# Kernel tuning notes

Measured on AMD Instinct MI355X. Metric: run time of the kernel, lower is better.

The kernel has to match this reference:

```python
import jax, jax.numpy as jnp
import numpy as np

N = 50000
E = 800000
IN_C = 128
HID = 64
HEADS = 4
OUT_C = 64


def setup_inputs() -> dict:
    key = jax.random.key(0)
    ks = jax.random.split(key, 20)
    s = 0.05
    inp = {
        "x": jax.random.normal(ks[0], (N, IN_C), dtype=jnp.float32),
        "edge_index": jax.random.randint(ks[1], (2, E), 0, N, dtype=jnp.int64),
        # layer 0: in=128 -> heads=4, C=64
        "W0": jax.random.normal(ks[2], (IN_C, HEADS * HID), jnp.float32) * s,
        "a0s": jax.random.normal(ks[3], (HEADS, HID), jnp.float32) * s,
        "a0d": jax.random.normal(ks[4], (HEADS, HID), jnp.float32) * s,
        "b0": jnp.zeros((HEADS * HID,), jnp.float32),
        # layer 1: 256 -> heads=4, C=64
        "W1": jax.random.normal(ks[5], (HEADS * HID, HEADS * HID), jnp.float32) * s,
        "a1s": jax.random.normal(ks[6], (HEADS, HID), jnp.float32) * s,
        "a1d": jax.random.normal(ks[7], (HEADS, HID), jnp.float32) * s,
        "b1": jnp.zeros((HEADS * HID,), jnp.float32),
        # layer 2: 256 -> heads=1, C=64
        "W2": jax.random.normal(ks[8], (HEADS * HID, HID), jnp.float32) * s,
        "a2s": jax.random.normal(ks[9], (1, HID), jnp.float32) * s,
        "a2d": jax.random.normal(ks[10], (1, HID), jnp.float32) * s,
        "b2": jnp.zeros((HID,), jnp.float32),
        # prediction head: Linear(64 -> 64)
        "hw": jax.random.normal(ks[11], (HID, OUT_C), jnp.float32) * s,
        "hb": jnp.zeros((OUT_C,), jnp.float32),
    }
    return inp


def gat_conv(x, src, dst, W, a_s, a_d, b, heads, n_nodes):
    # x: [N, F_in]; returns [N, heads*C]
    C = a_s.shape[1]
    h = (x @ W).reshape(n_nodes, heads, C)          # [N,H,C]
    alpha_s = jnp.sum(h * a_s, axis=-1)             # [N,H]
    alpha_d = jnp.sum(h * a_d, axis=-1)             # [N,H]
    e = jax.nn.leaky_relu(alpha_s[src] + alpha_d[dst], negative_slope=0.2)  # [E,H]
    m = jax.ops.segment_max(e, dst, num_segments=n_nodes)                  # per-dst max
    ex = jnp.exp(e - m[dst])
    denom = jax.ops.segment_sum(ex, dst, num_segments=n_nodes)
    alpha = ex / (denom[dst] + 1e-16)               # [E,H]
    out = jax.ops.segment_sum(alpha[:, :, None] * h[src], dst, num_segments=n_nodes)
    return out.reshape(n_nodes, heads * C) + b


def reference(x, edge_index, W0, a0s, a0d, b0, W1, a1s, a1d, b1, W2, a2s, a2d, b2, hw, hb):
    n = x.shape[0]
    # PyG GATConv default add_self_loops=True
    loop = jnp.arange(n, dtype=edge_index.dtype)
    src = jnp.concatenate([edge_index[0], loop])
    dst = jnp.concatenate([edge_index[1], loop])

    h = gat_conv(x, src, dst, W0, a0s, a0d, b0, HEADS, n)
    h = jax.nn.relu(h)
    h = gat_conv(h, src, dst, W1, a1s, a1d, b1, HEADS, n)
    h = jax.nn.relu(h)
    h = gat_conv(h, src, dst, W2, a2s, a2d, b2, 1, n)
    # batch is None -> mean over all nodes, keepdim
    g = jnp.mean(h, axis=0, keepdims=True)          # [1, HID]
    return g @ hw + hb                               # [1, OUT_C]
```

## Files before the change

### kernel.cpp

```cpp
#include <hip/hip_runtime.h>
#include <hip/hip_bf16.h>
#include <cstddef>

#define NN 50000
#define EE 800000
#define NB ((NN + 255) / 256)

typedef __attribute__((ext_vector_type(8))) short short8;
typedef __attribute__((ext_vector_type(4))) float f32x4;

__device__ __forceinline__ float leaky(float x) { return x >= 0.f ? x : 0.2f * x; }
__device__ __forceinline__ float bf2f(unsigned short u) {
  return __uint_as_float(((unsigned int)u) << 16);
}
__device__ __forceinline__ float bflo(unsigned int v) { return __uint_as_float(v << 16); }
__device__ __forceinline__ float bfhi(unsigned int v) { return __uint_as_float(v & 0xFFFF0000u); }
__device__ __forceinline__ unsigned short f2bf(float f) {
  __hip_bfloat16 b = __float2bfloat16(f);
  return __builtin_bit_cast(unsigned short, b);
}
__device__ __forceinline__ float selh(float4 v, int h) {
  float a = (h & 1) ? v.y : v.x;
  float b = (h & 1) ? v.w : v.z;
  return (h & 2) ? b : a;
}
__device__ __forceinline__ void accum8(float a, uint4 v, float* acc) {
  acc[0] += a * bflo(v.x); acc[1] += a * bfhi(v.x);
  acc[2] += a * bflo(v.y); acc[3] += a * bfhi(v.y);
  acc[4] += a * bflo(v.z); acc[5] += a * bfhi(v.z);
  acc[6] += a * bflo(v.w); acc[7] += a * bfhi(v.w);
}

__global__ __launch_bounds__(256) void gemm_bf16_k(const unsigned short* __restrict__ A,
                                                   const unsigned short* __restrict__ Bt,
                                                   unsigned short* __restrict__ Cb,
                                                   int K, int Nfull,
                                                   const float* __restrict__ a_s,
                                                   const float* __restrict__ a_d,
                                                   float* __restrict__ als,
                                                   float* __restrict__ ald,
                                                   float* __restrict__ selfex) {
  __shared__ __align__(16) unsigned short As[128 * 40];
  __shared__ __align__(16) unsigned short Bs[64 * 40];
  const int tid = threadIdx.x;
  const int lane = tid & 63;
  const int w = tid >> 6;
  const int bm = blockIdx.x * 128;
  const int bn = blockIdx.y * 64;
  const int quad = lane >> 4;
  const int l16 = lane & 15;
  f32x4 acc[2][4] = {};
  for (int kc = 0; kc < K; kc += 32) {
    {
      int row = tid >> 2, seg = tid & 3;
      int sr = bm + row; if (sr >= NN) sr = NN - 1;
      *(uint4*)&As[row * 40 + seg * 8] = *(const uint4*)(A + (size_t)sr * K + kc + seg * 8);
      row = (tid + 256) >> 2; seg = (tid + 256) & 3;
      sr = bm + row; if (sr >= NN) sr = NN - 1;
      *(uint4*)&As[row * 40 + seg * 8] = *(const uint4*)(A + (size_t)sr * K + kc + seg * 8);
      int n = tid >> 2; seg = tid & 3;
      *(uint4*)&Bs[n * 40 + seg * 8] = *(const uint4*)(Bt + (size_t)(bn + n) * K + kc + seg * 8);
    }
    __syncthreads();
    short8 afr0 = *(const short8*)&As[(w * 32 + l16) * 40 + quad * 8];
    short8 afr1 = *(const short8*)&As[(w * 32 + 16 + l16) * 40 + quad * 8];
#pragma unroll
    for (int nt = 0; nt < 4; ++nt) {
      short8 bfr = *(const short8*)&Bs[(nt * 16 + l16) * 40 + quad * 8];
      acc[0][nt] = __builtin_amdgcn_mfma_f32_16x16x32_bf16(afr0, bfr, acc[0][nt], 0, 0, 0);
      acc[1][nt] = __builtin_amdgcn_mfma_f32_16x16x32_bf16(afr1, bfr, acc[1][nt], 0, 0, 0);
    }
    __syncthreads();
  }
  const int head = bn >> 6;
  const int Hmul = Nfull >> 6;
  float vs[2][4] = {};
  float vd[2][4] = {};
#pragma unroll
  for (int nt = 0; nt < 4; ++nt) {
    const float asv = a_s[head * 64 + nt * 16 + l16];
    const float adv = a_d[head * 64 + nt * 16 + l16];
#pragma unroll
    for (int mt = 0; mt < 2; ++mt)
#pragma unroll
      for (int reg = 0; reg < 4; ++reg) {
        unsigned short c = f2bf(acc[mt][nt][reg]);
        int r = bm + w * 32 + mt * 16 + quad * 4 + reg;
        if (r < NN) Cb[(size_t)r * Nfull + bn + nt * 16 + l16] = c;
        float hv = bf2f(c);
        vs[mt][reg] += hv * asv;
        vd[mt][reg] += hv * adv;
      }
  }
#pragma unroll
  for (int off = 1; off < 16; off <<= 1) {
#pragma unroll
    for (int mt = 0; mt < 2; ++mt)
#pragma unroll
      for (int reg = 0; reg < 4; ++reg) {
        vs[mt][reg] += __shfl_xor(vs[mt][reg], off, 64);
        vd[mt][reg] += __shfl_xor(vd[mt][reg], off, 64);
      }
  }
  if (l16 == 0) {
#pragma unroll
    for (int mt = 0; mt < 2; ++mt)
#pragma unroll
      for (int reg = 0; reg < 4; ++reg) {
        int r = bm + w * 32 + mt * 16 + quad * 4 + reg;
        if (r < NN) {
          als[(size_t)r * Hmul + head] = vs[mt][reg];
          ald[(size_t)r * Hmul + head] = vd[mt][reg];
          selfex[(size_t)r * Hmul + head] = __expf(leaky(vs[mt][reg] + vd[mt][reg]));
        }
      }
  }
}

__global__ __launch_bounds__(256) void hist_k(const int* __restrict__ ei, int* deg) {
  int i = blockIdx.x * 256 + threadIdx.x;
  if (i < EE) atomicAdd(&deg[ei[EE + i]], 1);
}

__global__ __launch_bounds__(256) void scan1_k(const int* __restrict__ deg,
                                               int* __restrict__ incl,
                                               int* __restrict__ partial) {
  __shared__ int s[256];
  int t = threadIdx.x;
  int i = blockIdx.x * 256 + t;
  int v = (i < NN) ? deg[i] : 0;
  s[t] = v;
  __syncthreads();
  for (int off = 1; off < 256; off <<= 1) {
    int u = (t >= off) ? s[t - off] : 0;
    __syncthreads();
    s[t] += u;
    __syncthreads();
  }
  if (i < NN) incl[i] = s[t];
  if (t == 255) partial[blockIdx.x] = s[255];
}

__global__ void scan2_k(int* __restrict__ partial) {
  __shared__ int s[256];
  int t = threadIdx.x;
  int v = (t < NB) ? partial[t] : 0;
  s[t] = v;
  __syncthreads();
  for (int off = 1; off < 256; off <<= 1) {
    int u = (t >= off) ? s[t - off] : 0;
    __syncthreads();
    s[t] += u;
    __syncthreads();
  }
  if (t < NB) partial[t] = s[t] - v;
}

__global__ __launch_bounds__(256) void scan3_k(const int* __restrict__ deg,
                                               const int* __restrict__ incl,
                                               const int* __restrict__ partial,
                                               int* __restrict__ rowptr,
                                               int* __restrict__ cursor) {
  int i = blockIdx.x * 256 + threadIdx.x;
  if (i >= NN) return;
  int r = partial[blockIdx.x] + incl[i] - deg[i];
  rowptr[i] = r;
  cursor[i] = r;
}

__global__ __launch_bounds__(256) void scatter_k(const int* __restrict__ ei,
                                                 int* __restrict__ cursor,
                                                 int* __restrict__ csr_src,
                                                 int* __restrict__ csr_dst) {
  int i = blockIdx.x * 256 + threadIdx.x;
  if (i >= EE) return;
  int d = ei[EE + i];
  int p = atomicAdd(&cursor[d], 1);
  csr_src[p] = ei[i];
  csr_dst[p] = d;
}

__global__ __launch_bounds__(256) void edge_exp4_k(const int* __restrict__ csr_src,
                                                   const int* __restrict__ csr_dst,
                                                   const float* __restrict__ als,
                                                   const float* __restrict__ ald,
                                                   float4* __restrict__ ex4) {
  int i = blockIdx.x * 256 + threadIdx.x;
  if (i >= EE) return;
  int s = csr_src[i], d = csr_dst[i];
  const float4 as4 = *(const float4*)(als + (size_t)s * 4);
  const float4 ad4 = *(const float4*)(ald + (size_t)d * 4);
  float4 e;
  e.x = __expf(leaky(as4.x + ad4.x));
  e.y = __expf(leaky(as4.y + ad4.y));
  e.z = __expf(leaky(as4.z + ad4.z));
  e.w = __expf(leaky(as4.w + ad4.w));
  ex4[i] = e;
}

__global__ __launch_bounds__(256) void edge_exp1_k(const int* __restrict__ csr_src,
                                                   const int* __restrict__ csr_dst,
                                                   const float* __restrict__ als,
                                                   const float* __restrict__ ald,
                                                   float* __restrict__ ex1) {
  int i = blockIdx.x * 256 + threadIdx.x;
  if (i >= EE) return;
  ex1[i] = __expf(leaky(als[csr_src[i]] + ald[csr_dst[i]]));
}

__global__ __launch_bounds__(256) void aggr4c_k(const int* __restrict__ rowptr,
                                                const int* __restrict__ deg,
                                                const int* __restrict__ csr_src,
                                                const float4* __restrict__ ex4,
                                                const float* __restrict__ selfex,
                                                const uint4* __restrict__ hb4,
                                                const float* __restrict__ bias,
                                                uint4* __restrict__ out4) {
  const int dst = blockIdx.x * 4 + (threadIdx.x >> 6);
  const int lane = threadIdx.x & 63;
  const int slot = lane >> 4;
  const int l16 = lane & 15;
  const int head = l16 >> 2;
  const int rs = rowptr[dst];
  const int dg = deg[dst];

  float acc[16] = {};
  float dsum = 0.f;
  if (slot == 0) {
    float a = selfex[dst * 4 + head];
    dsum += a;
    uint4 v0 = hb4[(size_t)dst * 32 + l16 * 2];
    uint4 v1 = hb4[(size_t)dst * 32 + l16 * 2 + 1];
    accum8(a, v0, acc);
    accum8(a, v1, acc + 8);
  }
  int j = slot;
  for (; j + 4 < dg; j += 8) {
    int s0 = csr_src[rs + j];
    int s1 = csr_src[rs + j + 4];
    float4 av0 = ex4[rs + j];
    float4 av1 = ex4[rs + j + 4];
    uint4 va0 = hb4[(size_t)s0 * 32 + l16 * 2];
    uint4 vb0 = hb4[(size_t)s0 * 32 + l16 * 2 + 1];
    uint4 va1 = hb4[(size_t)s1 * 32 + l16 * 2];
    uint4 vb1 = hb4[(size_t)s1 * 32 + l16 * 2 + 1];
    float a0 = selh(av0, head);
    float a1 = selh(av1, head);
    dsum += a0 + a1;
    accum8(a0, va0, acc);
    accum8(a0, vb0, acc + 8);
    accum8(a1, va1, acc);
    accum8(a1, vb1, acc + 8);
  }
  for (; j < dg; j += 4) {
    int s0 = csr_src[rs + j];
    float4 av0 = ex4[rs + j];
    uint4 va0 = hb4[(size_t)s0 * 32 + l16 * 2];
    uint4 vb0 = hb4[(size_t)s0 * 32 + l16 * 2 + 1];
    float a0 = selh(av0, head);
    dsum += a0;
    accum8(a0, va0, acc);
    accum8(a0, vb0, acc + 8);
  }
#pragma unroll
  for (int k = 0; k < 16; ++k) {
    acc[k] += __shfl_xor(acc[k], 16, 64);
    acc[k] += __shfl_xor(acc[k], 32, 64);
  }
  dsum += __shfl_xor(dsum, 16, 64);
  dsum += __shfl_xor(dsum, 32, 64);
  if (slot == 0) {
    const float inv = 1.f / (dsum + 1e-16f);
    const float* bz = bias + l16 * 16;
    uint4 o0, o1;
    float c0, c1;
    c0 = fmaxf(acc[0] * inv + bz[0], 0.f);   c1 = fmaxf(acc[1] * inv + bz[1], 0.f);
    o0.x = ((unsigned int)f2bf(c1) << 16) | f2bf(c0);
    c0 = fmaxf(acc[2] * inv + bz[2], 0.f);   c1 = fmaxf(acc[3] * inv + bz[3], 0.f);
    o0.y = ((unsigned int)f2bf(c1) << 16) | f2bf(c0);
    c0 = fmaxf(acc[4] * inv + bz[4], 0.f);   c1 = fmaxf(acc[5] * inv + bz[5], 0.f);
    o0.z = ((unsigned int)f2bf(c1) << 16) | f2bf(c0);
    c0 = fmaxf(acc[6] * inv + bz[6], 0.f);   c1 = fmaxf(acc[7] * inv + bz[7], 0.f);
    o0.w = ((unsigned int)f2bf(c1) << 16) | f2bf(c0);
    c0 = fmaxf(acc[8] * inv + bz[8], 0.f);   c1 = fmaxf(acc[9] * inv + bz[9], 0.f);
    o1.x = ((unsigned int)f2bf(c1) << 16) | f2bf(c0);
    c0 = fmaxf(acc[10] * inv + bz[10], 0.f); c1 = fmaxf(acc[11] * inv + bz[11], 0.f);
    o1.y = ((unsigned int)f2bf(c1) << 16) | f2bf(c0);
    c0 = fmaxf(acc[12] * inv + bz[12], 0.f); c1 = fmaxf(acc[13] * inv + bz[13], 0.f);
    o1.z = ((unsigned int)f2bf(c1) << 16) | f2bf(c0);
    c0 = fmaxf(acc[14] * inv + bz[14], 0.f); c1 = fmaxf(acc[15] * inv + bz[15], 0.f);
    o1.w = ((unsigned int)f2bf(c1) << 16) | f2bf(c0);
    out4[(size_t)dst * 32 + l16 * 2] = o0;
    out4[(size_t)dst * 32 + l16 * 2 + 1] = o1;
  }
}

__global__ __launch_bounds__(256) void aggr1c_k(const int* __restrict__ rowptr,
                                                const int* __restrict__ deg,
                                                const int* __restrict__ csr_src,
                                                const float* __restrict__ ex1,
                                                const float* __restrict__ selfex,
                                                const uint4* __restrict__ hb4,
                                                const float* __restrict__ bias,
                                                float* __restrict__ out) {
  const int dst = blockIdx.x * 4 + (threadIdx.x >> 6);
  const int lane = threadIdx.x & 63;
  const int slot = lane >> 3;
  const int c8 = lane & 7;
  const int rs = rowptr[dst];
  const int dg = deg[dst];

  float acc[8] = {};
  float dsum = 0.f;
  if (slot == 0) {
    float a = selfex[dst];
    dsum += a;
    uint4 v = hb4[(size_t)dst * 8 + c8];
    accum8(a, v, acc);
  }
  for (int j = slot; j < dg; j += 8) {
    int s = csr_src[rs + j];
    float a = ex1[rs + j];
    dsum += a;
    uint4 v = hb4[(size_t)s * 8 + c8];
    accum8(a, v, acc);
  }
#pragma unroll
  for (int k = 0; k < 8; ++k) {
    acc[k] += __shfl_xor(acc[k], 8, 64);
    acc[k] += __shfl_xor(acc[k], 16, 64);
    acc[k] += __shfl_xor(acc[k], 32, 64);
  }
  dsum += __shfl_xor(dsum, 8, 64);
  dsum += __shfl_xor(dsum, 16, 64);
  dsum += __shfl_xor(dsum, 32, 64);
  if (slot == 0) {
    const float inv = 1.f / (dsum + 1e-16f);
    const float4 bz0 = *(const float4*)(bias + c8 * 8);
    const float4 bz1 = *(const float4*)(bias + c8 * 8 + 4);
    float4 o0 = make_float4(acc[0] * inv + bz0.x, acc[1] * inv + bz0.y,
                            acc[2] * inv + bz0.z, acc[3] * inv + bz0.w);
    float4 o1 = make_float4(acc[4] * inv + bz1.x, acc[5] * inv + bz1.y,
                            acc[6] * inv + bz1.z, acc[7] * inv + bz1.w);
    *(float4*)(out + (size_t)dst * 64 + c8 * 8) = o0;
    *(float4*)(out + (size_t)dst * 64 + c8 * 8 + 4) = o1;
  }
}

__global__ __launch_bounds__(256) void castx_k(const float2* __restrict__ x2,
                                               unsigned int* __restrict__ xb_u) {
  int i = blockIdx.x * 256 + threadIdx.x;
  if (i >= NN * 64) return;
  float2 v = x2[i];
  xb_u[i] = ((unsigned int)f2bf(v.y) << 16) | f2bf(v.x);
}

__global__ __launch_bounds__(64) void trw_k(const float* __restrict__ W,
                                            unsigned short* __restrict__ Wt, int K, int N) {
  int k = blockIdx.x;
  int n = blockIdx.y * 64 + threadIdx.x;
  Wt[(size_t)n * K + k] = f2bf(W[(size_t)k * N + n]);
}

__global__ __launch_bounds__(256) void colsum_k(const float* __restrict__ h2,
                                                float* __restrict__ g) {
  __shared__ float s[256];
  int tid = threadIdx.x;
  int c = tid & 63, rg = tid >> 6;
  float acc = 0.f;
  for (int n = blockIdx.x * 4 + rg; n < NN; n += gridDim.x * 4)
    acc += h2[n * 64 + c];
  s[tid] = acc;
  __syncthreads();
  if (tid < 64) atomicAdd(&g[c], s[c] + s[64 + c] + s[128 + c] + s[192 + c]);
}

__global__ void head_k(const float* __restrict__ g, const float* __restrict__ hw,
                       const float* __restrict__ hb, float* __restrict__ out) {
  int o = threadIdx.x;
  float acc = 0.f;
  const float invN = 1.0f / (float)NN;
#pragma unroll 8
  for (int c = 0; c < 64; ++c) acc += (g[c] * invN) * hw[c * 64 + o];
  out[o] = acc + hb[o];
}

extern "C" void kernel_launch(void* const* d_in, const int* in_sizes, int n_in,
                              void* d_out, int out_size, void* d_ws, size_t ws_size,
                              hipStream_t stream) {
  const float* x   = (const float*)d_in[0];
  const int*   ei  = (const int*)d_in[1];
  const float* W0  = (const float*)d_in[2];
  const float* a0s = (const float*)d_in[3];
  const float* a0d = (const float*)d_in[4];
  const float* b0  = (const float*)d_in[5];
  const float* W1  = (const float*)d_in[6];
  const float* a1s = (const float*)d_in[7];
  const float* a1d = (const float*)d_in[8];
  const float* b1  = (const float*)d_in[9];
  const float* W2  = (const float*)d_in[10];
  const float* a2s = (const float*)d_in[11];
  const float* a2d = (const float*)d_in[12];
  const float* b2  = (const float*)d_in[13];
  const float* hw  = (const float*)d_in[14];
  const float* hb  = (const float*)d_in[15];
  float* out = (float*)d_out;

  char* w = (char*)d_ws;
  unsigned short* xb   = (unsigned short*)w; w += (size_t)NN * 128 * 2;
  unsigned short* bufG = (unsigned short*)w; w += (size_t)NN * 256 * 2;
  unsigned short* bufA = (unsigned short*)w; w += (size_t)NN * 256 * 2;
  float* bufF = (float*)w;                   w += (size_t)NN * 64 * 4;
  unsigned short* W0t = (unsigned short*)w;  w += 256 * 128 * 2;
  unsigned short* W1t = (unsigned short*)w;  w += 256 * 256 * 2;
  unsigned short* W2t = (unsigned short*)w;  w += 64 * 256 * 2;
  float* als  = (float*)w;    w += (size_t)NN * 4 * 4;
  float* ald  = (float*)w;    w += (size_t)NN * 4 * 4;
  float* sfx  = (float*)w;    w += (size_t)NN * 4 * 4;
  float4* ex4 = (float4*)w;   w += (size_t)EE * 16;
  int* deg     = (int*)w;     w += (size_t)NN * 4;
  int* rowptr  = (int*)w;     w += (size_t)NN * 4;
  int* cursor  = (int*)w;     w += (size_t)NN * 4;
  int* incl    = (int*)w;     w += (size_t)NN * 4;
  int* partial = (int*)w;     w += 256 * 4;
  int* csr_src = (int*)w;     w += (size_t)EE * 4;
  int* csr_dst = (int*)w;     w += (size_t)EE * 4;
  float* g    = (float*)w;    w += 256;

  hipMemsetAsync(deg, 0, (size_t)NN * 4, stream);
  hist_k<<<(EE + 255) / 256, 256, 0, stream>>>(ei, deg);
  scan1_k<<<NB, 256, 0, stream>>>(deg, incl, partial);
  scan2_k<<<1, 256, 0, stream>>>(partial);
  scan3_k<<<NB, 256, 0, stream>>>(deg, incl, partial, rowptr, cursor);
  scatter_k<<<(EE + 255) / 256, 256, 0, stream>>>(ei, cursor, csr_src, csr_dst);

  castx_k<<<(NN * 64 + 255) / 256, 256, 0, stream>>>((const float2*)x, (unsigned int*)xb);
  trw_k<<<dim3(128, 4), 64, 0, stream>>>(W0, W0t, 128, 256);
  trw_k<<<dim3(256, 4), 64, 0, stream>>>(W1, W1t, 256, 256);
  trw_k<<<dim3(256, 1), 64, 0, stream>>>(W2, W2t, 256, 64);

  const int GX = (NN + 127) / 128;
  const int GA = NN / 4;
  const int GE = EE / 256;

  auto layer4 = [&](const unsigned short* in, int K, const unsigned short* Wt,
                    const float* a_s, const float* a_d, const float* bias,
                    unsigned short* hbuf, unsigned short* obuf) {
    gemm_bf16_k<<<dim3(GX, 4), 256, 0, stream>>>(in, Wt, hbuf, K, 256,
                                                 a_s, a_d, als, ald, sfx);
    edge_exp4_k<<<GE, 256, 0, stream>>>(csr_src, csr_dst, als, ald, ex4);
    aggr4c_k<<<GA, 256, 0, stream>>>(rowptr, deg, csr_src, ex4, sfx,
                                     (const uint4*)hbuf, bias, (uint4*)obuf);
  };

  layer4(xb, 128, W0t, a0s, a0d, b0, bufG, bufA);
  layer4(bufA, 256, W1t, a1s, a1d, b1, bufG, bufA);

  gemm_bf16_k<<<dim3(GX, 1), 256, 0, stream>>>(bufA, W2t, bufG, 256, 64,
                                               a2s, a2d, als, ald, sfx);
  edge_exp1_k<<<GE, 256, 0, stream>>>(csr_src, csr_dst, als, ald, (float*)ex4);
  aggr1c_k<<<GA, 256, 0, stream>>>(rowptr, deg, csr_src, (const float*)ex4, sfx,
                                   (const uint4*)bufG, b2, bufF);

  hipMemsetAsync(g, 0, 64 * 4, stream);
  colsum_k<<<256, 256, 0, stream>>>(bufF, g);
  head_k<<<1, 64, 0, stream>>>(g, hw, hb, out);
}
```

Measured before the change: 451.6 us.

## Deepen gather unrolling in aggregation kernels and fuse prep and head launches

Unrolls the 4-head aggregation loop from 2 to 4 edges per iteration and the 1-head loop from 1 to 2 edges, so more independent gathers are in flight per wave. Merges the x cast and three weight-transpose kernels into one prep kernel. Folds the final head matmul into the column-sum kernel using a last-block-done atomic counter, which removes launches at the cost of more registers and an extra fence.

Result: slower. 468.5 us (+3.7%).

```diff
diff --git a/kernel.cpp b/kernel.cpp
--- a/kernel.cpp
+++ b/kernel.cpp
@@ -235,22 +235,32 @@
     accum8(a, v1, acc + 8);
   }
   int j = slot;
-  for (; j + 4 < dg; j += 8) {
+  for (; j + 12 < dg; j += 16) {
     int s0 = csr_src[rs + j];
     int s1 = csr_src[rs + j + 4];
+    int s2 = csr_src[rs + j + 8];
+    int s3 = csr_src[rs + j + 12];
     float4 av0 = ex4[rs + j];
     float4 av1 = ex4[rs + j + 4];
+    float4 av2 = ex4[rs + j + 8];
+    float4 av3 = ex4[rs + j + 12];
     uint4 va0 = hb4[(size_t)s0 * 32 + l16 * 2];
     uint4 vb0 = hb4[(size_t)s0 * 32 + l16 * 2 + 1];
     uint4 va1 = hb4[(size_t)s1 * 32 + l16 * 2];
     uint4 vb1 = hb4[(size_t)s1 * 32 + l16 * 2 + 1];
+    uint4 va2 = hb4[(size_t)s2 * 32 + l16 * 2];
+    uint4 vb2 = hb4[(size_t)s2 * 32 + l16 * 2 + 1];
+    uint4 va3 = hb4[(size_t)s3 * 32 + l16 * 2];
+    uint4 vb3 = hb4[(size_t)s3 * 32 + l16 * 2 + 1];
     float a0 = selh(av0, head);
     float a1 = selh(av1, head);
-    dsum += a0 + a1;
-    accum8(a0, va0, acc);
-    accum8(a0, vb0, acc + 8);
-    accum8(a1, va1, acc);
-    accum8(a1, vb1, acc + 8);
+    float a2 = selh(av2, head);
+    float a3 = selh(av3, head);
+    dsum += (a0 + a1) + (a2 + a3);
+    accum8(a0, va0, acc); accum8(a0, vb0, acc + 8);
+    accum8(a1, va1, acc); accum8(a1, vb1, acc + 8);
+    accum8(a2, va2, acc); accum8(a2, vb2, acc + 8);
+    accum8(a3, va3, acc); accum8(a3, vb3, acc + 8);
   }
   for (; j < dg; j += 4) {
     int s0 = csr_src[rs + j];
@@ -318,11 +328,23 @@
     uint4 v = hb4[(size_t)dst * 8 + c8];
     accum8(a, v, acc);
   }
-  for (int j = slot; j < dg; j += 8) {
+  int j = slot;
+  for (; j + 8 < dg; j += 16) {
+    int s0 = csr_src[rs + j];
+    int s1 = csr_src[rs + j + 8];
+    float a0 = ex1[rs + j];
+    float a1 = ex1[rs + j + 8];
+    uint4 v0 = hb4[(size_t)s0 * 8 + c8];
+    uint4 v1 = hb4[(size_t)s1 * 8 + c8];
+    dsum += a0 + a1;
+    accum8(a0, v0, acc);
+    accum8(a1, v1, acc);
+  }
+  for (; j < dg; j += 8) {
     int s = csr_src[rs + j];
     float a = ex1[rs + j];
+    uint4 v = hb4[(size_t)s * 8 + c8];
     dsum += a;
-    uint4 v = hb4[(size_t)s * 8 + c8];
     accum8(a, v, acc);
   }
 #pragma unroll
@@ -347,24 +369,46 @@
   }
 }
 
-__global__ __launch_bounds__(256) void castx_k(const float2* __restrict__ x2,
-                                               unsigned int* __restrict__ xb_u) {
-  int i = blockIdx.x * 256 + threadIdx.x;
-  if (i >= NN * 64) return;
-  float2 v = x2[i];
-  xb_u[i] = ((unsigned int)f2bf(v.y) << 16) | f2bf(v.x);
-}
-
-__global__ __launch_bounds__(64) void trw_k(const float* __restrict__ W,
-                                            unsigned short* __restrict__ Wt, int K, int N) {
-  int k = blockIdx.x;
-  int n = blockIdx.y * 64 + threadIdx.x;
-  Wt[(size_t)n * K + k] = f2bf(W[(size_t)k * N + n]);
-}
-
-__global__ __launch_bounds__(256) void colsum_k(const float* __restrict__ h2,
-                                                float* __restrict__ g) {
+__global__ __launch_bounds__(256) void prep_k(const float2* __restrict__ x2,
+                                              unsigned int* __restrict__ xb_u,
+                                              const float* __restrict__ W0,
+                                              unsigned short* __restrict__ W0t,
+                                              const float* __restrict__ W1,
+                                              unsigned short* __restrict__ W1t,
+                                              const float* __restrict__ W2,
+                                              unsigned short* __restrict__ W2t) {
+  int bid = blockIdx.x;
+  int tid = threadIdx.x;
+  if (bid < 12500) {
+    int i = bid * 256 + tid;
+    float2 v = x2[i];
+    xb_u[i] = ((unsigned int)f2bf(v.y) << 16) | f2bf(v.x);
+    return;
+  }
+  int r = (bid - 12500) * 256 + tid;
+  if (r < 32768) {
+    int n = r >> 7, k = r & 127;
+    W0t[n * 128 + k] = f2bf(W0[k * 256 + n]);
+  } else if (r < 98304) {
+    int rr = r - 32768;
+    int n = rr >> 8, k = rr & 255;
+    W1t[n * 256 + k] = f2bf(W1[k * 256 + n]);
+  } else {
+    int rr = r - 98304;
+    int n = rr >> 8, k = rr & 255;
+    W2t[n * 256 + k] = f2bf(W2[k * 64 + n]);
+  }
+}
+
+__global__ __launch_bounds__(256) void colsum_head_k(const float* __restrict__ h2,
+                                                     float* __restrict__ g,
+                                                     unsigned int* __restrict__ cnt,
+                                                     const float* __restrict__ hw,
+                                                     const float* __restrict__ hb,
+                                                     float* __restrict__ out) {
   __shared__ float s[256];
+  __shared__ float sg[64];
+  __shared__ unsigned int sdone;
   int tid = threadIdx.x;
   int c = tid & 63, rg = tid >> 6;
   float acc = 0.f;
@@ -373,16 +417,20 @@
   s[tid] = acc;
   __syncthreads();
   if (tid < 64) atomicAdd(&g[c], s[c] + s[64 + c] + s[128 + c] + s[192 + c]);
-}
-
-__global__ void head_k(const float* __restrict__ g, const float* __restrict__ hw,
-                       const float* __restrict__ hb, float* __restrict__ out) {
-  int o = threadIdx.x;
-  float acc = 0.f;
-  const float invN = 1.0f / (float)NN;
+  __threadfence();
+  __syncthreads();
+  if (tid == 0) sdone = atomicAdd(cnt, 1);
+  __syncthreads();
+  if (sdone != gridDim.x - 1) return;
+  if (tid < 64) sg[tid] = atomicAdd(&g[tid], 0.f);
+  __syncthreads();
+  if (tid < 64) {
+    const float invN = 1.0f / (float)NN;
+    float a2 = hb[tid];
 #pragma unroll 8
-  for (int c = 0; c < 64; ++c) acc += (g[c] * invN) * hw[c * 64 + o];
-  out[o] = acc + hb[o];
+    for (int cc = 0; cc < 64; ++cc) a2 += sg[cc] * invN * hw[cc * 64 + tid];
+    out[tid] = a2;
+  }
 }
 
 extern "C" void kernel_launch(void* const* d_in, const int* in_sizes, int n_in,
@@ -434,10 +482,8 @@
   scan3_k<<<NB, 256, 0, stream>>>(deg, incl, partial, rowptr, cursor);
   scatter_k<<<(EE + 255) / 256, 256, 0, stream>>>(ei, cursor, csr_src, csr_dst);
 
-  castx_k<<<(NN * 64 + 255) / 256, 256, 0, stream>>>((const float2*)x, (unsigned int*)xb);
-  trw_k<<<dim3(128, 4), 64, 0, stream>>>(W0, W0t, 128, 256);
-  trw_k<<<dim3(256, 4), 64, 0, stream>>>(W1, W1t, 256, 256);
-  trw_k<<<dim3(256, 1), 64, 0, stream>>>(W2, W2t, 256, 64);
+  prep_k<<<12500 + 448, 256, 0, stream>>>((const float2*)x, (unsigned int*)xb,
+                                          W0, W0t, W1, W1t, W2, W2t);
 
   const int GX = (NN + 127) / 128;
   const int GA = NN / 4;
@@ -462,7 +508,6 @@
   aggr1c_k<<<GA, 256, 0, stream>>>(rowptr, deg, csr_src, (const float*)ex4, sfx,
                                    (const uint4*)bufG, b2, bufF);
 
-  hipMemsetAsync(g, 0, 64 * 4, stream);
-  colsum_k<<<256, 256, 0, stream>>>(bufF, g);
-  head_k<<<1, 64, 0, stream>>>(g, hw, hb, out);
-}
+  hipMemsetAsync(g, 0, 68 * 4, stream);
+  colsum_head_k<<<256, 256, 0, stream>>>(bufF, g, (unsigned int*)(g + 64), hw, hb, out);
+}
```
